# Optimization experiments

Measured on AMD Instinct MI355X. Metric: run time of the kernel, lower is better.

Reference implementation:

```python
import jax, jax.numpy as jnp
import numpy as np

D_MODEL = 256
N_HEADS = 8
N_LEVELS = 3
N_POINTS = 4
HEAD_DIM = D_MODEL // N_HEADS
SPATIAL_SHAPES = [(80, 80), (40, 40), (20, 20)]
B = 16
LEN_Q = 300
N_TOTAL = sum(h * w for h, w in SPATIAL_SHAPES)  # 8400
N_LP = N_LEVELS * N_POINTS


def setup_inputs() -> dict:
    key = jax.random.key(0)
    ks = jax.random.split(key, 8)
    s = 0.02
    return {
        "query": jax.random.normal(ks[0], (B, LEN_Q, D_MODEL), jnp.float32),
        "reference_points": jax.random.uniform(ks[1], (B, LEN_Q, N_LEVELS, 2), jnp.float32),
        "input_flatten": jax.random.normal(ks[2], (B, N_TOTAL, D_MODEL), jnp.float32),
        "W_off": jax.random.normal(ks[3], (D_MODEL, N_HEADS * N_LP * 2), jnp.float32) * s,
        "b_off": jnp.zeros((N_HEADS * N_LP * 2,), jnp.float32),
        "W_attn": jax.random.normal(ks[4], (D_MODEL, N_HEADS * N_LP), jnp.float32) * s,
        "b_attn": jnp.zeros((N_HEADS * N_LP,), jnp.float32),
        "W_val": jax.random.normal(ks[5], (D_MODEL, D_MODEL), jnp.float32) * s,
        "b_val": jnp.zeros((D_MODEL,), jnp.float32),
        "W_out": jax.random.normal(ks[6], (D_MODEL, D_MODEL), jnp.float32) * s,
        "b_out": jnp.zeros((D_MODEL,), jnp.float32),
    }


def _ms_deform_core(value, sampling_locations, attention_weights):
    # value: (B, n_heads, head_dim, N_total); locations: (B, Lq, H, L, P, 2) in [0,1]
    Bq, Lq = sampling_locations.shape[0], sampling_locations.shape[1]
    BN = Bq * N_HEADS
    grids = 2.0 * sampling_locations - 1.0
    starts = np.cumsum([0] + [h * w for h, w in SPATIAL_SHAPES])
    sampled_levels = []
    for lid, (H, W) in enumerate(SPATIAL_SHAPES):
        val_l = value[..., starts[lid]:starts[lid + 1]]                    # (B,H,hd,HW)
        val_flat = val_l.reshape(BN, HEAD_DIM, H * W).transpose(0, 2, 1)   # (BN,HW,hd)
        g = grids[:, :, :, lid].transpose(0, 2, 1, 3, 4).reshape(BN, Lq, N_POINTS, 2)
        ix = ((g[..., 0] + 1.0) * W - 1.0) / 2.0
        iy = ((g[..., 1] + 1.0) * H - 1.0) / 2.0
        ix0 = jnp.floor(ix).astype(jnp.int32)
        iy0 = jnp.floor(iy).astype(jnp.int32)
        ix1 = ix0 + 1
        iy1 = iy0 + 1
        fx = (ix - ix0.astype(ix.dtype))[..., None]
        fy = (iy - iy0.astype(iy.dtype))[..., None]

        def corner(iyc, ixc):
            valid = ((ixc >= 0) & (ixc < W) & (iyc >= 0) & (iyc < H)).astype(val_flat.dtype)
            idx = (jnp.clip(iyc, 0, H - 1) * W + jnp.clip(ixc, 0, W - 1))
            idx = idx.reshape(BN, Lq * N_POINTS, 1)
            v = jnp.take_along_axis(val_flat, idx, axis=1)
            return v.reshape(BN, Lq, N_POINTS, HEAD_DIM) * valid[..., None]

        v00 = corner(iy0, ix0)
        v01 = corner(iy0, ix1)
        v10 = corner(iy1, ix0)
        v11 = corner(iy1, ix1)
        sampled = ((1 - fx) * (1 - fy)) * v00 + (fx * (1 - fy)) * v01 \
                + ((1 - fx) * fy) * v10 + (fx * fy) * v11
        sampled_levels.append(sampled.transpose(0, 3, 1, 2))               # (BN,hd,Lq,P)
    sv = jnp.stack(sampled_levels, axis=-2).reshape(BN, HEAD_DIM, Lq, N_LP)
    a = attention_weights.transpose(0, 2, 1, 3).reshape(BN, 1, Lq, N_LP)
    out = jnp.sum(sv * a, axis=-1)                                         # (BN,hd,Lq)
    return out.reshape(Bq, D_MODEL, Lq).transpose(0, 2, 1)                 # (B,Lq,D)


def reference(query, reference_points, input_flatten,
              W_off, b_off, W_attn, b_attn, W_val, b_val, W_out, b_out):
    Bq, Lq = query.shape[0], query.shape[1]
    value = input_flatten @ W_val + b_val
    value = value.reshape(Bq, -1, N_HEADS, HEAD_DIM).transpose(0, 2, 3, 1)  # (B,H,hd,N)
    off = (query @ W_off + b_off).reshape(Bq, Lq, N_HEADS, N_LEVELS, N_POINTS, 2)
    attn = jax.nn.softmax((query @ W_attn + b_attn).reshape(Bq, Lq, N_HEADS, N_LP), axis=-1)
    # offset normalizer is (W,H) per level (x first)
    norm = jnp.array([[w, h] for h, w in SPATIAL_SHAPES], jnp.float32)
    loc = reference_points[:, :, None, :, None, :] + off / norm[None, None, None, :, None, :]
    out = _ms_deform_core(value, loc, attn)
    return out @ W_out + b_out
```

## Files before the change

kernel.cpp:

```cpp
#include <hip/hip_runtime.h>
#include <hip/hip_bf16.h>

#define DM 256
#define NH 8
#define HD 32
#define NLV 3
#define NPT 4
#define NLP 12
#define BB 16
#define LQ 300
#define NT 8400
#define MROWS (BB * NT)
#define QROWS (BB * LQ)
#define KP 40
#define KP2 72

typedef __bf16 bf16x8 __attribute__((ext_vector_type(8)));
typedef __bf16 bf16x4 __attribute__((ext_vector_type(4)));
typedef float  f32x16 __attribute__((ext_vector_type(16)));

__global__ void k_wt(const float* __restrict__ W_val,
                     const float* __restrict__ W_off,
                     const float* __restrict__ W_attn,
                     const float* __restrict__ W_out,
                     __hip_bfloat16* __restrict__ Wf,
                     __hip_bfloat16* __restrict__ Wt2,
                     __hip_bfloat16* __restrict__ Wt3)
{
    const int n = blockIdx.x;
    const int k = threadIdx.x;
    if (n < 256) {
        Wf[(size_t)(k >> 3) * 2048 + n * 8 + (k & 7)] =
            __float2bfloat16(W_val[(size_t)k * 256 + n]);
    } else if (n < 544) {
        const int n2 = n - 256;
        float v = (n2 < 192) ? W_off[(size_t)k * 192 + n2]
                             : W_attn[(size_t)k * 96 + (n2 - 192)];
        Wt2[(size_t)(k >> 5) * 9216 + n2 * 32 + (k & 31)] = __float2bfloat16(v);
    } else {
        const int n3 = n - 544;
        Wt3[(size_t)(k >> 5) * 8192 + n3 * 32 + (k & 31)] =
            __float2bfloat16(W_out[(size_t)k * 256 + n3]);
    }
}

__global__ __launch_bounds__(256) void k_valproj(
    const float* __restrict__ A,
    const __hip_bfloat16* __restrict__ Wf,
    const float* __restrict__ bias,
    __hip_bfloat16* __restrict__ V)
{
    __shared__ __hip_bfloat16 As[2][32 * KP2];

    const int t    = threadIdx.x;
    const int m0   = blockIdx.x * 32;
    const int wave = t >> 6;
    const int lane = t & 63;
    const int lm   = lane & 31;
    const int kh   = lane >> 5;
    const int lk   = kh * 8;

    f32x16 acc[2];
#pragma unroll
    for (int j = 0; j < 2; j++)
#pragma unroll
        for (int e = 0; e < 16; e++) acc[j][e] = 0.f;

    const int ar = t >> 3;
    const int ak = (t & 7) * 8;

    const __hip_bfloat16* wf0 = Wf + (size_t)(wave * 64 + lm) * 8 + kh * 2048;

    {
        const float* ap = A + (size_t)(m0 + ar) * 256 + ak;
        float4 a0 = *(const float4*)ap;
        float4 a1 = *(const float4*)(ap + 4);
        union { __hip_bfloat162 h2[4]; bf16x8 v; } ua;
        ua.h2[0] = __float22bfloat162_rn(make_float2(a0.x, a0.y));
        ua.h2[1] = __float22bfloat162_rn(make_float2(a0.z, a0.w));
        ua.h2[2] = __float22bfloat162_rn(make_float2(a1.x, a1.y));
        ua.h2[3] = __float22bfloat162_rn(make_float2(a1.z, a1.w));
        *(bf16x8*)(&As[0][ar * KP2 + ak]) = ua.v;
    }
    __syncthreads();

#pragma unroll
    for (int it = 0; it < 4; ++it) {
        const int buf = it & 1;
        float4 na0, na1;
        if (it < 3) {
            const float* ap = A + (size_t)(m0 + ar) * 256 + (it + 1) * 64 + ak;
            na0 = *(const float4*)ap;
            na1 = *(const float4*)(ap + 4);
        }
#pragma unroll
        for (int ks = 0; ks < 4; ++ks) {
            const int g = it * 4 + ks;
            bf16x8 af = *(const bf16x8*)(&As[buf][lm * KP2 + ks * 16 + lk]);
            bf16x8 b0 = *(const bf16x8*)(wf0 + (size_t)g * 4096);
            bf16x8 b1 = *(const bf16x8*)(wf0 + (size_t)g * 4096 + 256);
            acc[0] = __builtin_amdgcn_mfma_f32_32x32x16_bf16(af, b0, acc[0], 0, 0, 0);
            acc[1] = __builtin_amdgcn_mfma_f32_32x32x16_bf16(af, b1, acc[1], 0, 0, 0);
        }
        if (it < 3) {
            union { __hip_bfloat162 h2[4]; bf16x8 v; } ua;
            ua.h2[0] = __float22bfloat162_rn(make_float2(na0.x, na0.y));
            ua.h2[1] = __float22bfloat162_rn(make_float2(na0.z, na0.w));
            ua.h2[2] = __float22bfloat162_rn(make_float2(na1.x, na1.y));
            ua.h2[3] = __float22bfloat162_rn(make_float2(na1.z, na1.w));
            *(bf16x8*)(&As[buf ^ 1][ar * KP2 + ak]) = ua.v;
            __syncthreads();
        }
    }

#pragma unroll
    for (int j = 0; j < 2; j++) {
        const int n  = wave * 64 + j * 32 + lm;
        const float bn = bias[n];
        const int h  = n >> 5;
        const int d  = n & 31;
#pragma unroll
        for (int r = 0; r < 16; r++) {
            int rl = (r & 3) + 8 * (r >> 2) + 4 * kh;
            int m  = m0 + rl;
            int b  = m / NT;
            int pos = m - b * NT;
            V[((size_t)(b * NH + h) * NT + pos) * HD + d] =
                __float2bfloat16(acc[j][r] + bn);
        }
    }
}

__global__ __launch_bounds__(192) void k_offattn(
    const float* __restrict__ Q,
    const __hip_bfloat16* __restrict__ Wt2,
    const float* __restrict__ boff,
    const float* __restrict__ battn,
    float* __restrict__ off_out,
    float* __restrict__ attn_out)
{
    __shared__ __hip_bfloat16 As[32 * KP];
    __shared__ __hip_bfloat16 Ws[288 * KP];

    const int t    = threadIdx.x;
    const int m0   = blockIdx.x * 32;
    const int wave = t >> 6;
    const int lane = t & 63;
    const int lm   = lane & 31;
    const int lk   = (lane >> 5) * 8;

    f32x16 acc[3];
#pragma unroll
    for (int j = 0; j < 3; j++)
#pragma unroll
        for (int e = 0; e < 16; e++) acc[j][e] = 0.f;

    for (int kt = 0; kt < 256; kt += 32) {
        if (t < 128) {
            const int ar = t >> 2;
            const int ak = (t & 3) * 8;
            const float* ap = Q + (size_t)(m0 + ar) * 256 + kt + ak;
            float4 a0 = *(const float4*)ap;
            float4 a1 = *(const float4*)(ap + 4);
            union { __hip_bfloat162 h2[4]; bf16x8 v; } ua;
            ua.h2[0] = __float22bfloat162_rn(make_float2(a0.x, a0.y));
            ua.h2[1] = __float22bfloat162_rn(make_float2(a0.z, a0.w));
            ua.h2[2] = __float22bfloat162_rn(make_float2(a1.x, a1.y));
            ua.h2[3] = __float22bfloat162_rn(make_float2(a1.z, a1.w));
            *(bf16x8*)(As + ar * KP + ak) = ua.v;
        }
        {
            const __hip_bfloat16* wp = Wt2 + (size_t)(kt >> 5) * 9216 + t * 32;
            __hip_bfloat16* wd = Ws + t * KP;
            *(bf16x8*)(wd + 0)  = *(const bf16x8*)(wp + 0);
            *(bf16x8*)(wd + 8)  = *(const bf16x8*)(wp + 8);
            *(bf16x8*)(wd + 16) = *(const bf16x8*)(wp + 16);
            *(bf16x8*)(wd + 24) = *(const bf16x8*)(wp + 24);
            if (t < 96) {
                const __hip_bfloat16* wp2 = Wt2 + (size_t)(kt >> 5) * 9216 + (t + 192) * 32;
                __hip_bfloat16* wd2 = Ws + (t + 192) * KP;
                *(bf16x8*)(wd2 + 0)  = *(const bf16x8*)(wp2 + 0);
                *(bf16x8*)(wd2 + 8)  = *(const bf16x8*)(wp2 + 8);
                *(bf16x8*)(wd2 + 16) = *(const bf16x8*)(wp2 + 16);
                *(bf16x8*)(wd2 + 24) = *(const bf16x8*)(wp2 + 24);
            }
        }
        __syncthreads();

#pragma unroll
        for (int kk = 0; kk < 32; kk += 16) {
            bf16x8 af = *(const bf16x8*)(As + lm * KP + kk + lk);
#pragma unroll
            for (int j = 0; j < 3; j++) {
                bf16x8 bf = *(const bf16x8*)(Ws + (wave * 96 + j * 32 + lm) * KP + kk + lk);
                acc[j] = __builtin_amdgcn_mfma_f32_32x32x16_bf16(af, bf, acc[j], 0, 0, 0);
            }
        }
        __syncthreads();
    }

#pragma unroll
    for (int j = 0; j < 3; j++) {
        const int n = wave * 96 + j * 32 + lm;
        const float bias_ = (n < 192) ? boff[n] : battn[n - 192];
#pragma unroll
        for (int r = 0; r < 16; r++) {
            int rl = (r & 3) + 8 * (r >> 2) + 4 * (lane >> 5);
            int m  = m0 + rl;
            float v = acc[j][r] + bias_;
            if (n < 192) off_out[(size_t)m * 192 + n] = v;
            else         attn_out[(size_t)m * 96 + (n - 192)] = v;
        }
    }
}

__global__ __launch_bounds__(256) void k_sample(
    const float* __restrict__ off_raw,
    const float* __restrict__ attn_raw,
    const float* __restrict__ refp,
    const __hip_bfloat16* __restrict__ V,
    __hip_bfloat16* __restrict__ sampled)
{
    const int t  = threadIdx.x;
    const int q2 = t >> 7;
    const int tq = t & 127;
    const int bq = blockIdx.x * 2 + q2;
    const int b  = bq / LQ;

    __shared__ float aw[2][96];
    __shared__ float wc[2][96][4];
    __shared__ int   ic[2][96][4];

    if (tq < 8) {
        float v[12];
        float mx = -1e30f;
#pragma unroll
        for (int i = 0; i < 12; i++) {
            v[i] = attn_raw[(size_t)bq * 96 + tq * 12 + i];
            mx = fmaxf(mx, v[i]);
        }
        float s = 0.f;
#pragma unroll
        for (int i = 0; i < 12; i++) { v[i] = expf(v[i] - mx); s += v[i]; }
        float inv = 1.f / s;
#pragma unroll
        for (int i = 0; i < 12; i++) aw[q2][tq * 12 + i] = v[i] * inv;
    }
    __syncthreads();

    if (tq < 96) {
        const float dims[3]  = {80.f, 40.f, 20.f};
        const int startsl[3] = {0, 6400, 8000};
        const int idiml[3]   = {80, 40, 20};
        int h = tq / 12, lp = tq - h * 12, l = lp >> 2, p = lp & 3;
        float ox = off_raw[(size_t)bq * 192 + ((h * 3 + l) * 4 + p) * 2 + 0];
        float oy = off_raw[(size_t)bq * 192 + ((h * 3 + l) * 4 + p) * 2 + 1];
        float rx = refp[(size_t)bq * 6 + l * 2 + 0];
        float ry = refp[(size_t)bq * 6 + l * 2 + 1];
        float D  = dims[l];
        float lx = rx + ox / D;
        float ly = ry + oy / D;
        float ix = lx * D - 0.5f;
        float iy = ly * D - 0.5f;
        const int Dl = idiml[l];
        const int st = startsl[l];

        float fix = floorf(ix), fiy = floorf(iy);
        int ix0 = (int)fix, iy0 = (int)fiy;
        int ix1 = ix0 + 1, iy1 = iy0 + 1;
        float fx = ix - fix, fy = iy - fiy;

        float mx0 = (ix0 >= 0 && ix0 < Dl) ? 1.f : 0.f;
        float mx1 = (ix1 >= 0 && ix1 < Dl) ? 1.f : 0.f;
        float my0 = (iy0 >= 0 && iy0 < Dl) ? 1.f : 0.f;
        float my1 = (iy1 >= 0 && iy1 < Dl) ? 1.f : 0.f;

        int cx0 = min(max(ix0, 0), Dl - 1);
        int cx1 = min(max(ix1, 0), Dl - 1);
        int cy0 = min(max(iy0, 0), Dl - 1);
        int cy1 = min(max(iy1, 0), Dl - 1);

        float a = aw[q2][tq];
        wc[q2][tq][0] = (1.f - fx) * (1.f - fy) * mx0 * my0 * a;
        wc[q2][tq][1] = fx * (1.f - fy) * mx1 * my0 * a;
        wc[q2][tq][2] = (1.f - fx) * fy * mx0 * my1 * a;
        wc[q2][tq][3] = fx * fy * mx1 * my1 * a;
        ic[q2][tq][0] = (st + cy0 * Dl + cx0) * HD;
        ic[q2][tq][1] = (st + cy0 * Dl + cx1) * HD;
        ic[q2][tq][2] = (st + cy1 * Dl + cx0) * HD;
        ic[q2][tq][3] = (st + cy1 * Dl + cx1) * HD;
    }
    __syncthreads();

    const int h  = tq >> 4;
    const int dp = (tq & 15) * 2;
    const __hip_bfloat16* vb = V + (size_t)(b * NH + h) * NT * HD + dp;

    float acc0 = 0.f, acc1 = 0.f;
#pragma unroll
    for (int lp = 0; lp < 12; lp++) {
        const int s = h * 12 + lp;
        float4 w4 = *(const float4*)(&wc[q2][s][0]);
        int4   i4 = *(const int4*)(&ic[q2][s][0]);
        float2 v00 = __bfloat1622float2(*(const __hip_bfloat162*)(vb + i4.x));
        float2 v01 = __bfloat1622float2(*(const __hip_bfloat162*)(vb + i4.y));
        float2 v10 = __bfloat1622float2(*(const __hip_bfloat162*)(vb + i4.z));
        float2 v11 = __bfloat1622float2(*(const __hip_bfloat162*)(vb + i4.w));
        acc0 = fmaf(w4.x, v00.x, fmaf(w4.y, v01.x, fmaf(w4.z, v10.x, fmaf(w4.w, v11.x, acc0))));
        acc1 = fmaf(w4.x, v00.y, fmaf(w4.y, v01.y, fmaf(w4.z, v10.y, fmaf(w4.w, v11.y, acc1))));
    }
    *(__hip_bfloat162*)(sampled + (size_t)bq * 256 + h * 32 + dp) =
        __float22bfloat162_rn(make_float2(acc0, acc1));
}

__global__ __launch_bounds__(256) void k_outproj(
    const __hip_bfloat16* __restrict__ A,
    const __hip_bfloat16* __restrict__ Wt3,
    const float* __restrict__ bias,
    float* __restrict__ out)
{
    __shared__ __hip_bfloat16 As[32 * KP];
    __shared__ __hip_bfloat16 Ws[256 * KP];

    const int t    = threadIdx.x;
    const int m0   = blockIdx.x * 32;
    const int wave = t >> 6;
    const int lane = t & 63;
    const int lm   = lane & 31;
    const int lk   = (lane >> 5) * 8;

    f32x16 acc[2];
#pragma unroll
    for (int j = 0; j < 2; j++)
#pragma unroll
        for (int e = 0; e < 16; e++) acc[j][e] = 0.f;

    const int ar = t >> 3;
    const int ak = (t & 7) * 4;

    for (int kt = 0; kt < 256; kt += 32) {
        *(bf16x4*)(As + ar * KP + ak) =
            *(const bf16x4*)(A + (size_t)(m0 + ar) * 256 + kt + ak);
        {
            const __hip_bfloat16* wp = Wt3 + (size_t)(kt >> 5) * 8192 + t * 32;
            __hip_bfloat16* wd = Ws + t * KP;
            *(bf16x8*)(wd + 0)  = *(const bf16x8*)(wp + 0);
            *(bf16x8*)(wd + 8)  = *(const bf16x8*)(wp + 8);
            *(bf16x8*)(wd + 16) = *(const bf16x8*)(wp + 16);
            *(bf16x8*)(wd + 24) = *(const bf16x8*)(wp + 24);
        }
        __syncthreads();

#pragma unroll
        for (int kk = 0; kk < 32; kk += 16) {
            bf16x8 af = *(const bf16x8*)(As + lm * KP + kk + lk);
            bf16x8 bf0 = *(const bf16x8*)(Ws + (wave * 64 + 0 * 32 + lm) * KP + kk + lk);
            bf16x8 bf1 = *(const bf16x8*)(Ws + (wave * 64 + 1 * 32 + lm) * KP + kk + lk);
            acc[0] = __builtin_amdgcn_mfma_f32_32x32x16_bf16(af, bf0, acc[0], 0, 0, 0);
            acc[1] = __builtin_amdgcn_mfma_f32_32x32x16_bf16(af, bf1, acc[1], 0, 0, 0);
        }
        __syncthreads();
    }

#pragma unroll
    for (int j = 0; j < 2; j++) {
        const int n = wave * 64 + j * 32 + lm;
        const float bn = bias[n];
#pragma unroll
        for (int r = 0; r < 16; r++) {
            int rl = (r & 3) + 8 * (r >> 2) + 4 * (lane >> 5);
            int m  = m0 + rl;
            out[(size_t)m * 256 + n] = acc[j][r] + bn;
        }
    }
}

extern "C" void kernel_launch(void* const* d_in, const int* in_sizes, int n_in,
                              void* d_out, int out_size, void* d_ws, size_t ws_size,
                              hipStream_t stream) {
    const float* query  = (const float*)d_in[0];
    const float* refp   = (const float*)d_in[1];
    const float* inputf = (const float*)d_in[2];
    const float* W_off  = (const float*)d_in[3];
    const float* b_off  = (const float*)d_in[4];
    const float* W_attn = (const float*)d_in[5];
    const float* b_attn = (const float*)d_in[6];
    const float* W_val  = (const float*)d_in[7];
    const float* b_val  = (const float*)d_in[8];
    const float* W_out  = (const float*)d_in[9];
    const float* b_out  = (const float*)d_in[10];
    float* out = (float*)d_out;

    char* ws = (char*)d_ws;
    __hip_bfloat16* value   = (__hip_bfloat16*)ws;
    float* off_raw          = (float*)(ws + 68812800);
    float* attn_raw         = (float*)(ws + 72499200);
    __hip_bfloat16* sampled = (__hip_bfloat16*)(ws + 74342400);
    __hip_bfloat16* Wf      = (__hip_bfloat16*)(ws + 76800000);
    __hip_bfloat16* Wt2     = (__hip_bfloat16*)(ws + 76931072);
    __hip_bfloat16* Wt3     = (__hip_bfloat16*)(ws + 77078528);

    k_wt<<<800, 256, 0, stream>>>(W_val, W_off, W_attn, W_out, Wf, Wt2, Wt3);
    k_valproj<<<MROWS / 32, 256, 0, stream>>>(inputf, Wf, b_val, value);
    k_offattn<<<QROWS / 32, 192, 0, stream>>>(query, Wt2, b_off, b_attn,
                                              off_raw, attn_raw);
    k_sample<<<QROWS / 2, 256, 0, stream>>>(off_raw, attn_raw, refp, value, sampled);
    k_outproj<<<QROWS / 32, 256, 0, stream>>>(sampled, Wt3, b_out, out);
}
```

Baseline: 278.6 us.

## Merge value and offset/attention projections into one launch, remap sampling blocks per XCD

Combines the value projection and the offset/attention projection into a single kernel whose block range is split between the two GEMMs, removing one launch and letting the small query GEMM fill the tail of the large one. The offset/attention and output projections now read pre-fragmented weights directly from global memory with a double-buffered A tile, instead of staging full weight tiles in shared memory. The sampling kernel remaps block IDs so that each XCD handles whole batches, aiming for better L2 locality on the value tensor. In the merged kernel the offset/attention path leaves one of its four waves idle.

```diff
diff --git a/kernel.cpp b/kernel.cpp
--- a/kernel.cpp
+++ b/kernel.cpp
@@ -12,11 +12,9 @@
 #define NT 8400
 #define MROWS (BB * NT)
 #define QROWS (BB * LQ)
-#define KP 40
 #define KP2 72
 
 typedef __bf16 bf16x8 __attribute__((ext_vector_type(8)));
-typedef __bf16 bf16x4 __attribute__((ext_vector_type(4)));
 typedef float  f32x16 __attribute__((ext_vector_type(16)));
 
 __global__ void k_wt(const float* __restrict__ W_val,
@@ -24,8 +22,8 @@
                      const float* __restrict__ W_attn,
                      const float* __restrict__ W_out,
                      __hip_bfloat16* __restrict__ Wf,
-                     __hip_bfloat16* __restrict__ Wt2,
-                     __hip_bfloat16* __restrict__ Wt3)
+                     __hip_bfloat16* __restrict__ Wf2,
+                     __hip_bfloat16* __restrict__ Wf3)
 {
     const int n = blockIdx.x;
     const int k = threadIdx.x;
@@ -36,130 +34,50 @@
         const int n2 = n - 256;
         float v = (n2 < 192) ? W_off[(size_t)k * 192 + n2]
                              : W_attn[(size_t)k * 96 + (n2 - 192)];
-        Wt2[(size_t)(k >> 5) * 9216 + n2 * 32 + (k & 31)] = __float2bfloat16(v);
+        Wf2[(size_t)(k >> 3) * 2304 + n2 * 8 + (k & 7)] = __float2bfloat16(v);
     } else {
         const int n3 = n - 544;
-        Wt3[(size_t)(k >> 5) * 8192 + n3 * 32 + (k & 31)] =
+        Wf3[(size_t)(k >> 3) * 2048 + n3 * 8 + (k & 7)] =
             __float2bfloat16(W_out[(size_t)k * 256 + n3]);
     }
 }
 
-__global__ __launch_bounds__(256) void k_valproj(
+__global__ __launch_bounds__(256) void k_mm1(
     const float* __restrict__ A,
     const __hip_bfloat16* __restrict__ Wf,
-    const float* __restrict__ bias,
-    __hip_bfloat16* __restrict__ V)
+    const float* __restrict__ bval,
+    __hip_bfloat16* __restrict__ V,
+    const float* __restrict__ Q,
+    const __hip_bfloat16* __restrict__ Wf2,
+    const float* __restrict__ boff,
+    const float* __restrict__ battn,
+    float* __restrict__ off_out,
+    float* __restrict__ attn_out)
 {
     __shared__ __hip_bfloat16 As[2][32 * KP2];
 
     const int t    = threadIdx.x;
-    const int m0   = blockIdx.x * 32;
     const int wave = t >> 6;
     const int lane = t & 63;
     const int lm   = lane & 31;
     const int kh   = lane >> 5;
     const int lk   = kh * 8;
-
-    f32x16 acc[2];
-#pragma unroll
-    for (int j = 0; j < 2; j++)
-#pragma unroll
-        for (int e = 0; e < 16; e++) acc[j][e] = 0.f;
-
-    const int ar = t >> 3;
-    const int ak = (t & 7) * 8;
-
-    const __hip_bfloat16* wf0 = Wf + (size_t)(wave * 64 + lm) * 8 + kh * 2048;
-
-    {
-        const float* ap = A + (size_t)(m0 + ar) * 256 + ak;
-        float4 a0 = *(const float4*)ap;
-        float4 a1 = *(const float4*)(ap + 4);
-        union { __hip_bfloat162 h2[4]; bf16x8 v; } ua;
-        ua.h2[0] = __float22bfloat162_rn(make_float2(a0.x, a0.y));
-        ua.h2[1] = __float22bfloat162_rn(make_float2(a0.z, a0.w));
-        ua.h2[2] = __float22bfloat162_rn(make_float2(a1.x, a1.y));
-        ua.h2[3] = __float22bfloat162_rn(make_float2(a1.z, a1.w));
-        *(bf16x8*)(&As[0][ar * KP2 + ak]) = ua.v;
-    }
-    __syncthreads();
-
-#pragma unroll
-    for (int it = 0; it < 4; ++it) {
-        const int buf = it & 1;
-        float4 na0, na1;
-        if (it < 3) {
-            const float* ap = A + (size_t)(m0 + ar) * 256 + (it + 1) * 64 + ak;
-            na0 = *(const float4*)ap;
-            na1 = *(const float4*)(ap + 4);
-        }
-#pragma unroll
-        for (int ks = 0; ks < 4; ++ks) {
-            const int g = it * 4 + ks;
-            bf16x8 af = *(const bf16x8*)(&As[buf][lm * KP2 + ks * 16 + lk]);
-            bf16x8 b0 = *(const bf16x8*)(wf0 + (size_t)g * 4096);
-            bf16x8 b1 = *(const bf16x8*)(wf0 + (size_t)g * 4096 + 256);
-            acc[0] = __builtin_amdgcn_mfma_f32_32x32x16_bf16(af, b0, acc[0], 0, 0, 0);
-            acc[1] = __builtin_amdgcn_mfma_f32_32x32x16_bf16(af, b1, acc[1], 0, 0, 0);
-        }
-        if (it < 3) {
-            union { __hip_bfloat162 h2[4]; bf16x8 v; } ua;
-            ua.h2[0] = __float22bfloat162_rn(make_float2(na0.x, na0.y));
-            ua.h2[1] = __float22bfloat162_rn(make_float2(na0.z, na0.w));
-            ua.h2[2] = __float22bfloat162_rn(make_float2(na1.x, na1.y));
-            ua.h2[3] = __float22bfloat162_rn(make_float2(na1.z, na1.w));
-            *(bf16x8*)(&As[buf ^ 1][ar * KP2 + ak]) = ua.v;
-            __syncthreads();
-        }
-    }
-
-#pragma unroll
-    for (int j = 0; j < 2; j++) {
-        const int n  = wave * 64 + j * 32 + lm;
-        const float bn = bias[n];
-        const int h  = n >> 5;
-        const int d  = n & 31;
-#pragma unroll
-        for (int r = 0; r < 16; r++) {
-            int rl = (r & 3) + 8 * (r >> 2) + 4 * kh;
-            int m  = m0 + rl;
-            int b  = m / NT;
-            int pos = m - b * NT;
-            V[((size_t)(b * NH + h) * NT + pos) * HD + d] =
-                __float2bfloat16(acc[j][r] + bn);
-        }
-    }
-}
-
-__global__ __launch_bounds__(192) void k_offattn(
-    const float* __restrict__ Q,
-    const __hip_bfloat16* __restrict__ Wt2,
-    const float* __restrict__ boff,
-    const float* __restrict__ battn,
-    float* __restrict__ off_out,
-    float* __restrict__ attn_out)
-{
-    __shared__ __hip_bfloat16 As[32 * KP];
-    __shared__ __hip_bfloat16 Ws[288 * KP];
-
-    const int t    = threadIdx.x;
-    const int m0   = blockIdx.x * 32;
-    const int wave = t >> 6;
-    const int lane = t & 63;
-    const int lm   = lane & 31;
-    const int lk   = (lane >> 5) * 8;
-
-    f32x16 acc[3];
-#pragma unroll
-    for (int j = 0; j < 3; j++)
-#pragma unroll
-        for (int e = 0; e < 16; e++) acc[j][e] = 0.f;
-
-    for (int kt = 0; kt < 256; kt += 32) {
-        if (t < 128) {
-            const int ar = t >> 2;
-            const int ak = (t & 3) * 8;
-            const float* ap = Q + (size_t)(m0 + ar) * 256 + kt + ak;
+    const int ar   = t >> 3;
+    const int ak   = (t & 7) * 8;
+
+    if (blockIdx.x < MROWS / 32) {
+        const int m0 = blockIdx.x * 32;
+
+        f32x16 acc[2];
+#pragma unroll
+        for (int j = 0; j < 2; j++)
+#pragma unroll
+            for (int e = 0; e < 16; e++) acc[j][e] = 0.f;
+
+        const __hip_bfloat16* wf0 = Wf + (size_t)(wave * 64 + lm) * 8 + kh * 2048;
+
+        {
+            const float* ap = A + (size_t)(m0 + ar) * 256 + ak;
             float4 a0 = *(const float4*)ap;
             float4 a1 = *(const float4*)(ap + 4);
             union { __hip_bfloat162 h2[4]; bf16x8 v; } ua;
@@ -167,49 +85,125 @@
             ua.h2[1] = __float22bfloat162_rn(make_float2(a0.z, a0.w));
             ua.h2[2] = __float22bfloat162_rn(make_float2(a1.x, a1.y));
             ua.h2[3] = __float22bfloat162_rn(make_float2(a1.z, a1.w));
-            *(bf16x8*)(As + ar * KP + ak) = ua.v;
-        }
+            *(bf16x8*)(&As[0][ar * KP2 + ak]) = ua.v;
+        }
+        __syncthreads();
+
+#pragma unroll
+        for (int it = 0; it < 4; ++it) {
+            const int buf = it & 1;
+            float4 na0, na1;
+            if (it < 3) {
+                const float* ap = A + (size_t)(m0 + ar) * 256 + (it + 1) * 64 + ak;
+                na0 = *(const float4*)ap;
+                na1 = *(const float4*)(ap + 4);
+            }
+#pragma unroll
+            for (int ks = 0; ks < 4; ++ks) {
+                const int g = it * 4 + ks;
+                bf16x8 af = *(const bf16x8*)(&As[buf][lm * KP2 + ks * 16 + lk]);
+                bf16x8 b0 = *(const bf16x8*)(wf0 + (size_t)g * 4096);
+                bf16x8 b1 = *(const bf16x8*)(wf0 + (size_t)g * 4096 + 256);
+                acc[0] = __builtin_amdgcn_mfma_f32_32x32x16_bf16(af, b0, acc[0], 0, 0, 0);
+                acc[1] = __builtin_amdgcn_mfma_f32_32x32x16_bf16(af, b1, acc[1], 0, 0, 0);
+            }
+            if (it < 3) {
+                union { __hip_bfloat162 h2[4]; bf16x8 v; } ua;
+                ua.h2[0] = __float22bfloat162_rn(make_float2(na0.x, na0.y));
+                ua.h2[1] = __float22bfloat162_rn(make_float2(na0.z, na0.w));
+                ua.h2[2] = __float22bfloat162_rn(make_float2(na1.x, na1.y));
+                ua.h2[3] = __float22bfloat162_rn(make_float2(na1.z, na1.w));
+                *(bf16x8*)(&As[buf ^ 1][ar * KP2 + ak]) = ua.v;
+                __syncthreads();
+            }
+        }
+
+#pragma unroll
+        for (int j = 0; j < 2; j++) {
+            const int n  = wave * 64 + j * 32 + lm;
+            const float bn = bval[n];
+            const int h  = n >> 5;
+            const int d  = n & 31;
+#pragma unroll
+            for (int r = 0; r < 16; r++) {
+                int rl = (r & 3) + 8 * (r >> 2) + 4 * kh;
+                int m  = m0 + rl;
+                int b  = m / NT;
+                int pos = m - b * NT;
+                V[((size_t)(b * NH + h) * NT + pos) * HD + d] =
+                    __float2bfloat16(acc[j][r] + bn);
+            }
+        }
+    } else {
+        const int m0 = (blockIdx.x - MROWS / 32) * 32;
+
+        f32x16 acc[3];
+#pragma unroll
+        for (int j = 0; j < 3; j++)
+#pragma unroll
+            for (int e = 0; e < 16; e++) acc[j][e] = 0.f;
+
+        const __hip_bfloat16* wf0 = Wf2 + (size_t)(wave * 96 + lm) * 8 + kh * 2304;
+
         {
-            const __hip_bfloat16* wp = Wt2 + (size_t)(kt >> 5) * 9216 + t * 32;
-            __hip_bfloat16* wd = Ws + t * KP;
-            *(bf16x8*)(wd + 0)  = *(const bf16x8*)(wp + 0);
-            *(bf16x8*)(wd + 8)  = *(const bf16x8*)(wp + 8);
-            *(bf16x8*)(wd + 16) = *(const bf16x8*)(wp + 16);
-            *(bf16x8*)(wd + 24) = *(const bf16x8*)(wp + 24);
-            if (t < 96) {
-                const __hip_bfloat16* wp2 = Wt2 + (size_t)(kt >> 5) * 9216 + (t + 192) * 32;
-                __hip_bfloat16* wd2 = Ws + (t + 192) * KP;
-                *(bf16x8*)(wd2 + 0)  = *(const bf16x8*)(wp2 + 0);
-                *(bf16x8*)(wd2 + 8)  = *(const bf16x8*)(wp2 + 8);
-                *(bf16x8*)(wd2 + 16) = *(const bf16x8*)(wp2 + 16);
-                *(bf16x8*)(wd2 + 24) = *(const bf16x8*)(wp2 + 24);
-            }
+            const float* ap = Q + (size_t)(m0 + ar) * 256 + ak;
+            float4 a0 = *(const float4*)ap;
+            float4 a1 = *(const float4*)(ap + 4);
+            union { __hip_bfloat162 h2[4]; bf16x8 v; } ua;
+            ua.h2[0] = __float22bfloat162_rn(make_float2(a0.x, a0.y));
+            ua.h2[1] = __float22bfloat162_rn(make_float2(a0.z, a0.w));
+            ua.h2[2] = __float22bfloat162_rn(make_float2(a1.x, a1.y));
+            ua.h2[3] = __float22bfloat162_rn(make_float2(a1.z, a1.w));
+            *(bf16x8*)(&As[0][ar * KP2 + ak]) = ua.v;
         }
         __syncthreads();
 
 #pragma unroll
-        for (int kk = 0; kk < 32; kk += 16) {
-            bf16x8 af = *(const bf16x8*)(As + lm * KP + kk + lk);
+        for (int it = 0; it < 4; ++it) {
+            const int buf = it & 1;
+            float4 na0, na1;
+            if (it < 3) {
+                const float* ap = Q + (size_t)(m0 + ar) * 256 + (it + 1) * 64 + ak;
+                na0 = *(const float4*)ap;
+                na1 = *(const float4*)(ap + 4);
+            }
+#pragma unroll
+            for (int ks = 0; ks < 4; ++ks) {
+                const int g = it * 4 + ks;
+                bf16x8 af = *(const bf16x8*)(&As[buf][lm * KP2 + ks * 16 + lk]);
+                if (wave < 3) {
+#pragma unroll
+                    for (int j = 0; j < 3; j++) {
+                        bf16x8 bf = *(const bf16x8*)(wf0 + (size_t)g * 4608 + j * 256);
+                        acc[j] = __builtin_amdgcn_mfma_f32_32x32x16_bf16(af, bf, acc[j], 0, 0, 0);
+                    }
+                }
+            }
+            if (it < 3) {
+                union { __hip_bfloat162 h2[4]; bf16x8 v; } ua;
+                ua.h2[0] = __float22bfloat162_rn(make_float2(na0.x, na0.y));
+                ua.h2[1] = __float22bfloat162_rn(make_float2(na0.z, na0.w));
+                ua.h2[2] = __float22bfloat162_rn(make_float2(na1.x, na1.y));
+                ua.h2[3] = __float22bfloat162_rn(make_float2(na1.z, na1.w));
+                *(bf16x8*)(&As[buf ^ 1][ar * KP2 + ak]) = ua.v;
+                __syncthreads();
+            }
+        }
+
+        if (wave < 3) {
 #pragma unroll
             for (int j = 0; j < 3; j++) {
-                bf16x8 bf = *(const bf16x8*)(Ws + (wave * 96 + j * 32 + lm) * KP + kk + lk);
-                acc[j] = __builtin_amdgcn_mfma_f32_32x32x16_bf16(af, bf, acc[j], 0, 0, 0);
-            }
-        }
-        __syncthreads();
-    }
-
-#pragma unroll
-    for (int j = 0; j < 3; j++) {
-        const int n = wave * 96 + j * 32 + lm;
-        const float bias_ = (n < 192) ? boff[n] : battn[n - 192];
-#pragma unroll
-        for (int r = 0; r < 16; r++) {
-            int rl = (r & 3) + 8 * (r >> 2) + 4 * (lane >> 5);
-            int m  = m0 + rl;
-            float v = acc[j][r] + bias_;
-            if (n < 192) off_out[(size_t)m * 192 + n] = v;
-            else         attn_out[(size_t)m * 96 + (n - 192)] = v;
+                const int n = wave * 96 + j * 32 + lm;
+                const float bias_ = (n < 192) ? boff[n] : battn[n - 192];
+#pragma unroll
+                for (int r = 0; r < 16; r++) {
+                    int rl = (r & 3) + 8 * (r >> 2) + 4 * kh;
+                    int m  = m0 + rl;
+                    float v = acc[j][r] + bias_;
+                    if (n < 192) off_out[(size_t)m * 192 + n] = v;
+                    else         attn_out[(size_t)m * 96 + (n - 192)] = v;
+                }
+            }
         }
     }
 }
@@ -224,8 +218,13 @@
     const int t  = threadIdx.x;
     const int q2 = t >> 7;
     const int tq = t & 127;
-    const int bq = blockIdx.x * 2 + q2;
-    const int b  = bq / LQ;
+
+    const int bid  = blockIdx.x;
+    const int xcd  = bid & 7;
+    const int slot = bid >> 3;
+    const int hi   = (slot >= 150) ? 1 : 0;
+    const int b    = xcd + (hi << 3);
+    const int bq   = b * LQ + (slot - hi * 150) * 2 + q2;
 
     __shared__ float aw[2][96];
     __shared__ float wc[2][96][4];
@@ -315,19 +314,21 @@
 
 __global__ __launch_bounds__(256) void k_outproj(
     const __hip_bfloat16* __restrict__ A,
-    const __hip_bfloat16* __restrict__ Wt3,
+    const __hip_bfloat16* __restrict__ Wf3,
     const float* __restrict__ bias,
     float* __restrict__ out)
 {
-    __shared__ __hip_bfloat16 As[32 * KP];
-    __shared__ __hip_bfloat16 Ws[256 * KP];
+    __shared__ __hip_bfloat16 As[2][32 * KP2];
 
     const int t    = threadIdx.x;
     const int m0   = blockIdx.x * 32;
     const int wave = t >> 6;
     const int lane = t & 63;
     const int lm   = lane & 31;
-    const int lk   = (lane >> 5) * 8;
+    const int kh   = lane >> 5;
+    const int lk   = kh * 8;
+    const int ar   = t >> 3;
+    const int ak   = (t & 7) * 8;
 
     f32x16 acc[2];
 #pragma unroll
@@ -335,31 +336,31 @@
 #pragma unroll
         for (int e = 0; e < 16; e++) acc[j][e] = 0.f;
 
-    const int ar = t >> 3;
-    const int ak = (t & 7) * 4;
-
-    for (int kt = 0; kt < 256; kt += 32) {
-        *(bf16x4*)(As + ar * KP + ak) =
-            *(const bf16x4*)(A + (size_t)(m0 + ar) * 256 + kt + ak);
-        {
-            const __hip_bfloat16* wp = Wt3 + (size_t)(kt >> 5) * 8192 + t * 32;
-            __hip_bfloat16* wd = Ws + t * KP;
-            *(bf16x8*)(wd + 0)  = *(const bf16x8*)(wp + 0);
-            *(bf16x8*)(wd + 8)  = *(const bf16x8*)(wp + 8);
-            *(bf16x8*)(wd + 16) = *(const bf16x8*)(wp + 16);
-            *(bf16x8*)(wd + 24) = *(const bf16x8*)(wp + 24);
-        }
-        __syncthreads();
-
-#pragma unroll
-        for (int kk = 0; kk < 32; kk += 16) {
-            bf16x8 af = *(const bf16x8*)(As + lm * KP + kk + lk);
-            bf16x8 bf0 = *(const bf16x8*)(Ws + (wave * 64 + 0 * 32 + lm) * KP + kk + lk);
-            bf16x8 bf1 = *(const bf16x8*)(Ws + (wave * 64 + 1 * 32 + lm) * KP + kk + lk);
-            acc[0] = __builtin_amdgcn_mfma_f32_32x32x16_bf16(af, bf0, acc[0], 0, 0, 0);
-            acc[1] = __builtin_amdgcn_mfma_f32_32x32x16_bf16(af, bf1, acc[1], 0, 0, 0);
-        }
-        __syncthreads();
+    const __hip_bfloat16* wf0 = Wf3 + (size_t)(wave * 64 + lm) * 8 + kh * 2048;
+
+    *(bf16x8*)(&As[0][ar * KP2 + ak]) =
+        *(const bf16x8*)(A + (size_t)(m0 + ar) * 256 + ak);
+    __syncthreads();
+
+#pragma unroll
+    for (int it = 0; it < 4; ++it) {
+        const int buf = it & 1;
+        bf16x8 na;
+        if (it < 3)
+            na = *(const bf16x8*)(A + (size_t)(m0 + ar) * 256 + (it + 1) * 64 + ak);
+#pragma unroll
+        for (int ks = 0; ks < 4; ++ks) {
+            const int g = it * 4 + ks;
+            bf16x8 af = *(const bf16x8*)(&As[buf][lm * KP2 + ks * 16 + lk]);
+            bf16x8 b0 = *(const bf16x8*)(wf0 + (size_t)g * 4096);
+            bf16x8 b1 = *(const bf16x8*)(wf0 + (size_t)g * 4096 + 256);
+            acc[0] = __builtin_amdgcn_mfma_f32_32x32x16_bf16(af, b0, acc[0], 0, 0, 0);
+            acc[1] = __builtin_amdgcn_mfma_f32_32x32x16_bf16(af, b1, acc[1], 0, 0, 0);
+        }
+        if (it < 3) {
+            *(bf16x8*)(&As[buf ^ 1][ar * KP2 + ak]) = na;
+            __syncthreads();
+        }
     }
 
 #pragma unroll
@@ -368,7 +369,7 @@
         const float bn = bias[n];
 #pragma unroll
         for (int r = 0; r < 16; r++) {
-            int rl = (r & 3) + 8 * (r >> 2) + 4 * (lane >> 5);
+            int rl = (r & 3) + 8 * (r >> 2) + 4 * kh;
             int m  = m0 + rl;
             out[(size_t)m * 256 + n] = acc[j][r] + bn;
         }
@@ -397,13 +398,12 @@
     float* attn_raw         = (float*)(ws + 72499200);
     __hip_bfloat16* sampled = (__hip_bfloat16*)(ws + 74342400);
     __hip_bfloat16* Wf      = (__hip_bfloat16*)(ws + 76800000);
-    __hip_bfloat16* Wt2     = (__hip_bfloat16*)(ws + 76931072);
-    __hip_bfloat16* Wt3     = (__hip_bfloat16*)(ws + 77078528);
-
-    k_wt<<<800, 256, 0, stream>>>(W_val, W_off, W_attn, W_out, Wf, Wt2, Wt3);
-    k_valproj<<<MROWS / 32, 256, 0, stream>>>(inputf, Wf, b_val, value);
-    k_offattn<<<QROWS / 32, 192, 0, stream>>>(query, Wt2, b_off, b_attn,
-                                              off_raw, attn_raw);
+    __hip_bfloat16* Wf2     = (__hip_bfloat16*)(ws + 76931072);
+    __hip_bfloat16* Wf3     = (__hip_bfloat16*)(ws + 77078528);
+
+    k_wt<<<800, 256, 0, stream>>>(W_val, W_off, W_attn, W_out, Wf, Wf2, Wf3);
+    k_mm1<<<MROWS / 32 + QROWS / 32, 256, 0, stream>>>(
+        inputf, Wf, b_val, value, query, Wf2, b_off, b_attn, off_raw, attn_raw);
     k_sample<<<QROWS / 2, 256, 0, stream>>>(off_raw, attn_raw, refp, value, sampled);
-    k_outproj<<<QROWS / 32, 256, 0, stream>>>(sampled, Wt3, b_out, out);
+    k_outproj<<<QROWS / 32, 256, 0, stream>>>(sampled, Wf3, b_out, out);
 }
```

Measured after the change: 267.4 us. 4.0% less time.
